# Performance work log

Hardware: AMD Instinct MI355X
Metric: run time of the kernel (lower is better)

## Reference

```python
import jax, jax.numpy as jnp
import numpy as np

N = 1_000_000   # number of points (voxels)
C = 64          # number of instance clusters
D = 3           # embedding / coordinate dimension

EMBEDDING_WEIGHT = 1.0
SEEDINESS_WEIGHT = 1.0
SMOOTHING_WEIGHT = 1.0


def setup_inputs() -> dict:
    key = jax.random.key(0)
    k1, k2, k3, k4, k5 = jax.random.split(key, 5)
    embeddings = jax.random.normal(k1, (N, D), dtype=jnp.float32)
    margins = jax.random.uniform(k2, (N, 1), dtype=jnp.float32)
    seediness = jax.random.uniform(k3, (N, 1), dtype=jnp.float32)
    coords = jax.random.uniform(k4, (N, D), dtype=jnp.float32)
    labels = jax.random.randint(k5, (N,), 0, C, dtype=jnp.int32)
    return {
        "embeddings": embeddings,
        "margins": margins,
        "seediness": seediness,
        "coords": coords,
        "labels": labels,
        "num_clusters": C,
    }


def reference(embeddings, margins, seediness, coords, labels, num_clusters):
    Nc = num_clusters
    n = labels.shape[0]
    ones = jnp.ones((n,), embeddings.dtype)
    counts = jax.ops.segment_sum(ones, labels, num_segments=Nc)            # (C,)
    # per-cluster centroid of COORDS (find_cluster_means(coords, labels))
    centroids = jax.ops.segment_sum(coords, labels, num_segments=Nc) / counts[:, None]  # (C,D)
    # per-cluster sigma = mean of margins over cluster members -> (C,1)
    sigma = jax.ops.segment_sum(margins, labels, num_segments=Nc) / counts[:, None]

    # squared distance of every point to every centroid, (C,N), via GEMM expansion
    e_sq = jnp.sum(embeddings * embeddings, axis=1)                 # (N,)
    c_sq = jnp.sum(centroids * centroids, axis=1)                   # (C,)
    dists = c_sq[:, None] + e_sq[None, :] - 2.0 * (centroids @ embeddings.T)  # (C,N)

    # gaussian kernel probability, clamped to [0,1]
    p = jnp.clip(jnp.exp(-dists / (2.0 * sigma * sigma)), 0.0, 1.0)  # (C,N), sigma (C,1) broadcasts

    mask = (labels[None, :] == jnp.arange(Nc, dtype=labels.dtype)[:, None]).astype(p.dtype)  # (C,N)

    # StableBCELoss(p, mask): clamp(x,0) - x*t + log(1+exp(-|x|)), mean per cluster,
    # then averaged over clusters == global mean since every row has N elements.
    bce = jnp.clip(p, 0.0, None) - p * mask + jnp.log1p(jnp.exp(-jnp.abs(p)))
    mask_loss = jnp.mean(bce)

    # probs[n] = p[label_n, n]
    probs = p[labels, jnp.arange(n)]                                # (N,)

    # smoothing: sum over cluster members of (margin - sigma.detach())^2, averaged over clusters
    sigma_det = jax.lax.stop_gradient(sigma)                        # (C,1)
    smoothing_loss = jnp.sum((margins - sigma_det[labels]) ** 2) / Nc

    # seediness: L1 between detached probs and seediness prediction
    seed_loss = jnp.mean(jnp.abs(jax.lax.stop_gradient(probs) - seediness[:, 0]))

    total_loss = (EMBEDDING_WEIGHT * mask_loss
                  + SEEDINESS_WEIGHT * seed_loss
                  + SMOOTHING_WEIGHT * smoothing_loss)
    return total_loss
```

## Files before the change

kernel.cpp:

```cpp
#include <hip/hip_runtime.h>
#include <math.h>

#define NCLUS 64
#define BLOCK 256
#define GC 512
#define NREP 8
#define FP_SCALE 1048576.0f

#if __has_builtin(__builtin_amdgcn_exp2f)
#define EXP2F(x) __builtin_amdgcn_exp2f(x)
#else
#define EXP2F(x) __expf(0.6931471805599453f * (x))
#endif

#define SPQ0 0.692941
#define SPQ1 0.503668f
#define SPQ2 0.117225f


__global__ void init_ws_kernel(unsigned long long* S8) {
    int i = blockIdx.x * blockDim.x + threadIdx.x;
    if (i < NREP * 5 * NCLUS) S8[i] = 0ULL;
}

__global__ __launch_bounds__(BLOCK) void cluster_sums_kernel(
        const float* __restrict__ coords, const float* __restrict__ margins,
        const int* __restrict__ labels, int n, unsigned long long* __restrict__ S8) {
    __shared__ float s_h[8][5][65];
    for (int i = threadIdx.x; i < 8 * 5 * 65; i += BLOCK)
        ((float*)s_h)[i] = 0.0f;
    __syncthreads();

    const int rep = threadIdx.x & 7;
    const int np = n >> 1;
    const int stride = gridDim.x * BLOCK;
    const float2* c2 = (const float2*)coords;
    const float2* m2 = (const float2*)margins;
    const int2* l2 = (const int2*)labels;

    for (int i = blockIdx.x * BLOCK + threadIdx.x; i < np; i += stride) {
        float2 a0 = c2[i * 3], a1 = c2[i * 3 + 1], a2 = c2[i * 3 + 2];
        float2 mg = m2[i];
        int2 lb = l2[i];
        atomicAdd(&s_h[rep][0][lb.x], 1.0f);
        atomicAdd(&s_h[rep][1][lb.x], a0.x);
        atomicAdd(&s_h[rep][2][lb.x], a0.y);
        atomicAdd(&s_h[rep][3][lb.x], a1.x);
        atomicAdd(&s_h[rep][4][lb.x], mg.x);
        atomicAdd(&s_h[rep][0][lb.y], 1.0f);
        atomicAdd(&s_h[rep][1][lb.y], a1.y);
        atomicAdd(&s_h[rep][2][lb.y], a2.x);
        atomicAdd(&s_h[rep][3][lb.y], a2.y);
        atomicAdd(&s_h[rep][4][lb.y], mg.y);
    }
    if ((n & 1) && blockIdx.x == 0 && threadIdx.x == 0) {
        int p = n - 1;
        int lab = labels[p];
        atomicAdd(&s_h[rep][0][lab], 1.0f);
        atomicAdd(&s_h[rep][1][lab], coords[p * 3 + 0]);
        atomicAdd(&s_h[rep][2][lab], coords[p * 3 + 1]);
        atomicAdd(&s_h[rep][3][lab], coords[p * 3 + 2]);
        atomicAdd(&s_h[rep][4][lab], margins[p]);
    }
    __syncthreads();

    unsigned long long* Sr = S8 + (blockIdx.x & (NREP - 1)) * 5 * NCLUS;
    for (int idx = threadIdx.x; idx < 5 * NCLUS; idx += BLOCK) {
        int field = idx >> 6, c = idx & 63;
        float v = 0.0f;
#pragma unroll
        for (int r = 0; r < 8; ++r) v += s_h[r][field][c];
        unsigned long long q = (unsigned long long)(long long)llrintf(v * FP_SCALE);
        if (q) atomicAdd(&Sr[idx], q);
    }
}

__device__ __forceinline__ float block_reduce_f(float v, float* s_red) {
    for (int o = 32; o > 0; o >>= 1) v += __shfl_down(v, o);
    int lane = threadIdx.x & 63, wid = threadIdx.x >> 6;
    __syncthreads();
    if (lane == 0) s_red[wid] = v;
    __syncthreads();
    float t = 0.0f;
    if (threadIdx.x == 0)
        for (int w = 0; w < BLOCK / 64; ++w) t += s_red[w];
    return t;
}

__global__ __launch_bounds__(BLOCK, 8) void main_loss_kernel(
        const float* __restrict__ emb, const float* __restrict__ margins,
        const float* __restrict__ seed, const int* __restrict__ labels,
        int n, const unsigned long long* __restrict__ S8,
        float* __restrict__ pb) {
    __shared__ float4 s_par[NCLUS];
    __shared__ float s_w[NCLUS];
    __shared__ float s_sig[NCLUS];
    __shared__ float s_red[BLOCK / 64];

    if (threadIdx.x < NCLUS) {
        int c = threadIdx.x;
        long long acc[5] = {0, 0, 0, 0, 0};
#pragma unroll
        for (int r = 0; r < NREP; ++r) {
#pragma unroll
            for (int f = 0; f < 5; ++f)
                acc[f] += (long long)S8[r * 5 * NCLUS + f * NCLUS + c];
        }
        float cnt = (float)acc[0];
        float sx = (float)acc[1], sy = (float)acc[2], sz = (float)acc[3];
        float sm = (float)acc[4];
        float inv = 1.0f / cnt;
        float sig = sm * inv;
        float cx = sx * inv, cy = sy * inv, cz = sz * inv;
        float w2 = -1.4426950408889634f / (2.0f * sig * sig);
        s_par[c] = make_float4(-2.0f * w2 * cx, -2.0f * w2 * cy, -2.0f * w2 * cz,
                               w2 * fmaf(cx, cx, fmaf(cy, cy, cz * cz)));
        s_w[c] = w2;
        s_sig[c] = sig;
    }
    __syncthreads();

    const int np = n >> 1;
    const int i = blockIdx.x * BLOCK + threadIdx.x;

    float bce = 0.0f, seed_s = 0.0f, smooth_s = 0.0f;

    if (i < np) {
        const float2* e2 = (const float2*)emb;
        float2 a0 = e2[i * 3], a1 = e2[i * 3 + 1], a2 = e2[i * 3 + 2];
        float2 mg = ((const float2*)margins)[i];
        float2 sv = ((const float2*)seed)[i];
        int2 lb = ((const int2*)labels)[i];

        float x[2] = {a0.x, a1.y};
        float y[2] = {a0.y, a2.x};
        float z[2] = {a1.x, a2.y};
        float es[2], a[2] = {0.f, 0.f};
#pragma unroll
        for (int k = 0; k < 2; ++k)
            es[k] = fmaf(x[k], x[k], fmaf(y[k], y[k], z[k] * z[k]));

#pragma unroll 8
        for (int c = 0; c < NCLUS; ++c) {
            float4 pr = s_par[c];
            float w2 = s_w[c];
#pragma unroll
            for (int k = 0; k < 2; ++k) {
                float t = fmaf(pr.x, x[k], fmaf(pr.y, y[k],
                          fmaf(pr.z, z[k], fmaf(w2, es[k], pr.w))));
                float p = EXP2F(t);
                a[k] = fmaf(p, fmaf(p, SPQ2, SPQ1), a[k]);
            }
        }
        bce += a[0] + a[1];

        float mm[2] = {mg.x, mg.y};
        float ss[2] = {sv.x, sv.y};
        int   ll[2] = {lb.x, lb.y};
#pragma unroll
        for (int k = 0; k < 2; ++k) {
            float4 pr = s_par[ll[k]];
            float w2 = s_w[ll[k]];
            float t = fmaf(pr.x, x[k], fmaf(pr.y, y[k],
                      fmaf(pr.z, z[k], fmaf(w2, es[k], pr.w))));
            float p = EXP2F(t);
            bce -= p;
            seed_s += fabsf(p - ss[k]);
            float dg = mm[k] - s_sig[ll[k]];
            smooth_s += dg * dg;
        }
    }
    if ((n & 1) && blockIdx.x == 0 && threadIdx.x == 0) {
        int p = n - 1;
        float ex = emb[p * 3 + 0], ey = emb[p * 3 + 1], ez = emb[p * 3 + 2];
        float esq = fmaf(ex, ex, fmaf(ey, ey, ez * ez));
        int lab = labels[p];
        float pl = 0.0f;
        for (int c = 0; c < NCLUS; ++c) {
            float4 pr = s_par[c];
            float w2 = s_w[c];
            float t = fmaf(pr.x, ex, fmaf(pr.y, ey, fmaf(pr.z, ez, fmaf(w2, esq, pr.w))));
            float p2 = EXP2F(t);
            pl = (c == lab) ? p2 : pl;
            bce = fmaf(p2, fmaf(p2, SPQ2, SPQ1), bce);
        }
        bce -= pl;
        seed_s += fabsf(pl - seed[p]);
        float dg = margins[p] - s_sig[lab];
        smooth_s += dg * dg;
    }

    float r;
    r = block_reduce_f(bce, s_red);
    if (threadIdx.x == 0) pb[blockIdx.x * 3 + 0] = r;
    r = block_reduce_f(seed_s, s_red);
    if (threadIdx.x == 0) pb[blockIdx.x * 3 + 1] = r;
    r = block_reduce_f(smooth_s, s_red);
    if (threadIdx.x == 0) pb[blockIdx.x * 3 + 2] = r;
}

__global__ void finalize_kernel(const float* __restrict__ pb, int nb,
                                float* __restrict__ out, int n) {
    __shared__ float s_red[BLOCK / 64];
    float v0 = 0.f, v1 = 0.f, v2 = 0.f;
    for (int j = threadIdx.x; j < nb; j += BLOCK) {
        v0 += pb[j * 3 + 0];
        v1 += pb[j * 3 + 1];
        v2 += pb[j * 3 + 2];
    }
    float t0 = block_reduce_f(v0, s_red);
    __syncthreads();
    float t1 = block_reduce_f(v1, s_red);
    __syncthreads();
    float t2 = block_reduce_f(v2, s_red);
    if (threadIdx.x == 0) {
        double bce_total = (double)t0 + (double)n * 64.0 * SPQ0;
        out[0] = (float)(bce_total / ((double)NCLUS * (double)n)
                         + (double)t1 / (double)n + (double)t2 / (double)NCLUS);
    }
}

extern "C" void kernel_launch(void* const* d_in, const int* in_sizes, int n_in,
                              void* d_out, int out_size, void* d_ws, size_t ws_size,
                              hipStream_t stream) {
    const float* emb     = (const float*)d_in[0];
    const float* margins = (const float*)d_in[1];
    const float* seed    = (const float*)d_in[2];
    const float* coords  = (const float*)d_in[3];
    const int*   labels  = (const int*)d_in[4];
    int n = in_sizes[4];

    unsigned long long* S8 = (unsigned long long*)d_ws;
    float* pb = (float*)((char*)d_ws + 24576);
    float* out = (float*)d_out;

    int np = n >> 1;
    int grid_main = (np + BLOCK - 1) / BLOCK;
    if (grid_main < 1) grid_main = 1;
    int grid_cs = grid_main < GC ? grid_main : GC;

    init_ws_kernel<<<(NREP * 5 * NCLUS + 255) / 256, 256, 0, stream>>>(S8);
    cluster_sums_kernel<<<grid_cs, BLOCK, 0, stream>>>(coords, margins, labels, n, S8);
    main_loss_kernel<<<grid_main, BLOCK, 0, stream>>>(emb, margins, seed, labels, n, S8, pb);
    finalize_kernel<<<1, BLOCK, 0, stream>>>(pb, grid_main, out, n);
}
```

Before: 59.38 us.

## Precompute cluster params in separate kernel and read them via scalar loads

Moves the per-cluster parameter computation (centroid, sigma, Gaussian coefficients) out of every main-loss block into a single tiny kernel that writes them to workspace. The main kernel then reads these uniform values directly from global memory, which the compiler can turn into scalar loads, instead of each block recomputing them from the 8-replica sums and staging them in shared memory behind a barrier. This removes the redundant per-block reduction and the LDS traffic in the 64-cluster inner loop. The cost is one extra kernel launch and global or cached loads in place of LDS reads.

```diff
diff --git a/kernel.cpp b/kernel.cpp
--- a/kernel.cpp
+++ b/kernel.cpp
@@ -75,30 +75,10 @@
     }
 }
 
-__device__ __forceinline__ float block_reduce_f(float v, float* s_red) {
-    for (int o = 32; o > 0; o >>= 1) v += __shfl_down(v, o);
-    int lane = threadIdx.x & 63, wid = threadIdx.x >> 6;
-    __syncthreads();
-    if (lane == 0) s_red[wid] = v;
-    __syncthreads();
-    float t = 0.0f;
-    if (threadIdx.x == 0)
-        for (int w = 0; w < BLOCK / 64; ++w) t += s_red[w];
-    return t;
-}
-
-__global__ __launch_bounds__(BLOCK, 8) void main_loss_kernel(
-        const float* __restrict__ emb, const float* __restrict__ margins,
-        const float* __restrict__ seed, const int* __restrict__ labels,
-        int n, const unsigned long long* __restrict__ S8,
-        float* __restrict__ pb) {
-    __shared__ float4 s_par[NCLUS];
-    __shared__ float s_w[NCLUS];
-    __shared__ float s_sig[NCLUS];
-    __shared__ float s_red[BLOCK / 64];
-
-    if (threadIdx.x < NCLUS) {
-        int c = threadIdx.x;
+__global__ void compute_params_kernel(const unsigned long long* __restrict__ S8,
+                                      float* __restrict__ P) {
+    int c = threadIdx.x;
+    if (c < NCLUS) {
         long long acc[5] = {0, 0, 0, 0, 0};
 #pragma unroll
         for (int r = 0; r < NREP; ++r) {
@@ -113,12 +93,34 @@
         float sig = sm * inv;
         float cx = sx * inv, cy = sy * inv, cz = sz * inv;
         float w2 = -1.4426950408889634f / (2.0f * sig * sig);
-        s_par[c] = make_float4(-2.0f * w2 * cx, -2.0f * w2 * cy, -2.0f * w2 * cz,
-                               w2 * fmaf(cx, cx, fmaf(cy, cy, cz * cz)));
-        s_w[c] = w2;
-        s_sig[c] = sig;
-    }
-    __syncthreads();
+        ((float4*)P)[c] = make_float4(-2.0f * w2 * cx, -2.0f * w2 * cy,
+                                      -2.0f * w2 * cz,
+                                      w2 * fmaf(cx, cx, fmaf(cy, cy, cz * cz)));
+        P[256 + c] = w2;
+        P[320 + c] = sig;
+    }
+}
+
+__device__ __forceinline__ float block_reduce_f(float v, float* s_red) {
+    for (int o = 32; o > 0; o >>= 1) v += __shfl_down(v, o);
+    int lane = threadIdx.x & 63, wid = threadIdx.x >> 6;
+    __syncthreads();
+    if (lane == 0) s_red[wid] = v;
+    __syncthreads();
+    float t = 0.0f;
+    if (threadIdx.x == 0)
+        for (int w = 0; w < BLOCK / 64; ++w) t += s_red[w];
+    return t;
+}
+
+__global__ __launch_bounds__(BLOCK, 8) void main_loss_kernel(
+        const float* __restrict__ emb, const float* __restrict__ margins,
+        const float* __restrict__ seed, const int* __restrict__ labels,
+        int n, const float* __restrict__ P, float* __restrict__ pb) {
+    __shared__ float s_red[BLOCK / 64];
+    const float4* __restrict__ P4 = (const float4*)P;
+    const float* __restrict__ Pw = P + 256;
+    const float* __restrict__ Psig = P + 320;
 
     const int np = n >> 1;
     const int i = blockIdx.x * BLOCK + threadIdx.x;
@@ -142,8 +144,8 @@
 
 #pragma unroll 8
         for (int c = 0; c < NCLUS; ++c) {
-            float4 pr = s_par[c];
-            float w2 = s_w[c];
+            float4 pr = P4[c];
+            float w2 = Pw[c];
 #pragma unroll
             for (int k = 0; k < 2; ++k) {
                 float t = fmaf(pr.x, x[k], fmaf(pr.y, y[k],
@@ -159,14 +161,15 @@
         int   ll[2] = {lb.x, lb.y};
 #pragma unroll
         for (int k = 0; k < 2; ++k) {
-            float4 pr = s_par[ll[k]];
-            float w2 = s_w[ll[k]];
+            float4 pr = P4[ll[k]];
+            float w2 = Pw[ll[k]];
+            float sg = Psig[ll[k]];
             float t = fmaf(pr.x, x[k], fmaf(pr.y, y[k],
                       fmaf(pr.z, z[k], fmaf(w2, es[k], pr.w))));
             float p = EXP2F(t);
             bce -= p;
             seed_s += fabsf(p - ss[k]);
-            float dg = mm[k] - s_sig[ll[k]];
+            float dg = mm[k] - sg;
             smooth_s += dg * dg;
         }
     }
@@ -177,8 +180,8 @@
         int lab = labels[p];
         float pl = 0.0f;
         for (int c = 0; c < NCLUS; ++c) {
-            float4 pr = s_par[c];
-            float w2 = s_w[c];
+            float4 pr = P4[c];
+            float w2 = Pw[c];
             float t = fmaf(pr.x, ex, fmaf(pr.y, ey, fmaf(pr.z, ez, fmaf(w2, esq, pr.w))));
             float p2 = EXP2F(t);
             pl = (c == lab) ? p2 : pl;
@@ -186,7 +189,7 @@
         }
         bce -= pl;
         seed_s += fabsf(pl - seed[p]);
-        float dg = margins[p] - s_sig[lab];
+        float dg = margins[p] - Psig[lab];
         smooth_s += dg * dg;
     }
 
@@ -231,6 +234,7 @@
     int n = in_sizes[4];
 
     unsigned long long* S8 = (unsigned long long*)d_ws;
+    float* P  = (float*)((char*)d_ws + 20480);
     float* pb = (float*)((char*)d_ws + 24576);
     float* out = (float*)d_out;
 
@@ -241,6 +245,7 @@
 
     init_ws_kernel<<<(NREP * 5 * NCLUS + 255) / 256, 256, 0, stream>>>(S8);
     cluster_sums_kernel<<<grid_cs, BLOCK, 0, stream>>>(coords, margins, labels, n, S8);
-    main_loss_kernel<<<grid_main, BLOCK, 0, stream>>>(emb, margins, seed, labels, n, S8, pb);
+    compute_params_kernel<<<1, 64, 0, stream>>>(S8, P);
+    main_loss_kernel<<<grid_main, BLOCK, 0, stream>>>(emb, margins, seed, labels, n, P, pb);
     finalize_kernel<<<1, BLOCK, 0, stream>>>(pb, grid_main, out, n);
 }
```

Measured after the change: 60.97 us. +2.7%, slower.

## Replace fixed-point global atomics with per-block slots and a single params kernel

Applied to the files above, without the earlier changes.

Cluster-sum blocks now write their float partial sums to private global slots instead of doing 64-bit fixed-point atomics, which also removes the workspace zeroing kernel. A new single-block kernel reduces the 512 slots and computes the per-cluster Gaussian parameters once. Each main-kernel block then loads those precomputed parameters instead of re-reducing the replicas and redoing the divisions. This adds a serial single-block reduction over about 160K floats and changes the summation order, which can slightly change the float results.

```diff
diff --git a/kernel.cpp b/kernel.cpp
--- a/kernel.cpp
+++ b/kernel.cpp
@@ -4,8 +4,7 @@
 #define NCLUS 64
 #define BLOCK 256
 #define GC 512
-#define NREP 8
-#define FP_SCALE 1048576.0f
+#define FP_FIELDS 320
 
 #if __has_builtin(__builtin_amdgcn_exp2f)
 #define EXP2F(x) __builtin_amdgcn_exp2f(x)
@@ -18,14 +17,9 @@
 #define SPQ2 0.117225f
 
 
-__global__ void init_ws_kernel(unsigned long long* S8) {
-    int i = blockIdx.x * blockDim.x + threadIdx.x;
-    if (i < NREP * 5 * NCLUS) S8[i] = 0ULL;
-}
-
 __global__ __launch_bounds__(BLOCK) void cluster_sums_kernel(
         const float* __restrict__ coords, const float* __restrict__ margins,
-        const int* __restrict__ labels, int n, unsigned long long* __restrict__ S8) {
+        const int* __restrict__ labels, int n, float* __restrict__ slots) {
     __shared__ float s_h[8][5][65];
     for (int i = threadIdx.x; i < 8 * 5 * 65; i += BLOCK)
         ((float*)s_h)[i] = 0.0f;
@@ -64,14 +58,48 @@
     }
     __syncthreads();
 
-    unsigned long long* Sr = S8 + (blockIdx.x & (NREP - 1)) * 5 * NCLUS;
-    for (int idx = threadIdx.x; idx < 5 * NCLUS; idx += BLOCK) {
+    float* slot = slots + blockIdx.x * FP_FIELDS;
+    for (int idx = threadIdx.x; idx < FP_FIELDS; idx += BLOCK) {
         int field = idx >> 6, c = idx & 63;
         float v = 0.0f;
 #pragma unroll
         for (int r = 0; r < 8; ++r) v += s_h[r][field][c];
-        unsigned long long q = (unsigned long long)(long long)llrintf(v * FP_SCALE);
-        if (q) atomicAdd(&Sr[idx], q);
+        slot[idx] = v;
+    }
+}
+
+__global__ __launch_bounds__(512) void compute_params_kernel(
+        const float* __restrict__ slots, int nb, float* __restrict__ P) {
+    __shared__ float s_p[8][5][64];
+    const int c = threadIdx.x & 63;
+    const int g = threadIdx.x >> 6;
+
+    float acc[5] = {0.f, 0.f, 0.f, 0.f, 0.f};
+    for (int b = g; b < nb; b += 8) {
+        const float* slot = slots + b * FP_FIELDS;
+#pragma unroll
+        for (int f = 0; f < 5; ++f) acc[f] += slot[f * 64 + c];
+    }
+#pragma unroll
+    for (int f = 0; f < 5; ++f) s_p[g][f][c] = acc[f];
+    __syncthreads();
+
+    if (threadIdx.x < NCLUS) {
+        float cnt = 0.f, sx = 0.f, sy = 0.f, sz = 0.f, sm = 0.f;
+#pragma unroll
+        for (int r = 0; r < 8; ++r) {
+            cnt += s_p[r][0][c]; sx += s_p[r][1][c]; sy += s_p[r][2][c];
+            sz += s_p[r][3][c]; sm += s_p[r][4][c];
+        }
+        float inv = 1.0f / cnt;
+        float sig = sm * inv;
+        float cx = sx * inv, cy = sy * inv, cz = sz * inv;
+        float w2 = -1.4426950408889634f / (2.0f * sig * sig);
+        ((float4*)P)[c] = make_float4(-2.0f * w2 * cx, -2.0f * w2 * cy,
+                                      -2.0f * w2 * cz,
+                                      w2 * fmaf(cx, cx, fmaf(cy, cy, cz * cz)));
+        P[256 + c] = w2;
+        P[320 + c] = sig;
     }
 }
 
@@ -90,8 +118,7 @@
 __global__ __launch_bounds__(BLOCK, 8) void main_loss_kernel(
         const float* __restrict__ emb, const float* __restrict__ margins,
         const float* __restrict__ seed, const int* __restrict__ labels,
-        int n, const unsigned long long* __restrict__ S8,
-        float* __restrict__ pb) {
+        int n, const float* __restrict__ P, float* __restrict__ pb) {
     __shared__ float4 s_par[NCLUS];
     __shared__ float s_w[NCLUS];
     __shared__ float s_sig[NCLUS];
@@ -99,24 +126,9 @@
 
     if (threadIdx.x < NCLUS) {
         int c = threadIdx.x;
-        long long acc[5] = {0, 0, 0, 0, 0};
-#pragma unroll
-        for (int r = 0; r < NREP; ++r) {
-#pragma unroll
-            for (int f = 0; f < 5; ++f)
-                acc[f] += (long long)S8[r * 5 * NCLUS + f * NCLUS + c];
-        }
-        float cnt = (float)acc[0];
-        float sx = (float)acc[1], sy = (float)acc[2], sz = (float)acc[3];
-        float sm = (float)acc[4];
-        float inv = 1.0f / cnt;
-        float sig = sm * inv;
-        float cx = sx * inv, cy = sy * inv, cz = sz * inv;
-        float w2 = -1.4426950408889634f / (2.0f * sig * sig);
-        s_par[c] = make_float4(-2.0f * w2 * cx, -2.0f * w2 * cy, -2.0f * w2 * cz,
-                               w2 * fmaf(cx, cx, fmaf(cy, cy, cz * cz)));
-        s_w[c] = w2;
-        s_sig[c] = sig;
+        s_par[c] = ((const float4*)P)[c];
+        s_w[c] = P[256 + c];
+        s_sig[c] = P[320 + c];
     }
     __syncthreads();
 
@@ -230,8 +242,9 @@
     const int*   labels  = (const int*)d_in[4];
     int n = in_sizes[4];
 
-    unsigned long long* S8 = (unsigned long long*)d_ws;
-    float* pb = (float*)((char*)d_ws + 24576);
+    float* slots = (float*)d_ws;
+    float* P  = (float*)((char*)d_ws + 655360);
+    float* pb = (float*)((char*)d_ws + 657408);
     float* out = (float*)d_out;
 
     int np = n >> 1;
@@ -239,8 +252,8 @@
     if (grid_main < 1) grid_main = 1;
     int grid_cs = grid_main < GC ? grid_main : GC;
 
-    init_ws_kernel<<<(NREP * 5 * NCLUS + 255) / 256, 256, 0, stream>>>(S8);
-    cluster_sums_kernel<<<grid_cs, BLOCK, 0, stream>>>(coords, margins, labels, n, S8);
-    main_loss_kernel<<<grid_main, BLOCK, 0, stream>>>(emb, margins, seed, labels, n, S8, pb);
+    cluster_sums_kernel<<<grid_cs, BLOCK, 0, stream>>>(coords, margins, labels, n, slots);
+    compute_params_kernel<<<1, 512, 0, stream>>>(slots, grid_cs, P);
+    main_loss_kernel<<<grid_main, BLOCK, 0, stream>>>(emb, margins, seed, labels, n, P, pb);
     finalize_kernel<<<1, BLOCK, 0, stream>>>(pb, grid_main, out, n);
 }
```

Measured after the change: 71.90 us. 1.21x slower.
